# Kernel tuning notes

Hardware: AMD Instinct MI355X
Metric: run time of the kernel (lower is better)

Reference implementation:

```python
import jax, jax.numpy as jnp
import numpy as np

TEMPERATURE = 0.1
N = 8192
V = 2
D = 512

def setup_inputs() -> dict:
    key = jax.random.key(0)
    k1, k2, k3 = jax.random.split(key, 3)
    features = jax.random.normal(k1, (N, V, D), dtype=jnp.float32)
    features1 = jax.random.normal(k2, (N, V, D), dtype=jnp.float32)
    y = jax.random.randint(k3, (N,), 0, 10, dtype=jnp.int64)
    return {"features": features, "features1": features1, "y": y}

def reference(features, features1, y):
    # Take view 0; L2-normalize anchors only (features1 is NOT normalized in the original).
    anchor = features[:, 0, :]
    anchor = anchor / jnp.linalg.norm(anchor, axis=1, keepdims=True)
    f1 = features1[:, 0, :]
    # sim: [N, N]
    sim = jnp.einsum('nd,md->nm', anchor, f1)
    # Original builds logits = [diag_i | row_i without diag] / T and uses label 0.
    # That concat is a permutation of the full row, so
    # CE(row) = logsumexp(row / T) - diag / T, averaged over rows.
    logits = sim / TEMPERATURE
    pos = jnp.diagonal(logits)  # [N]
    loss = jnp.mean(jax.nn.logsumexp(logits, axis=1) - pos)
    return loss
```

## Files before the change

### kernel.cpp

```cpp
#include <hip/hip_runtime.h>
#include <hip/hip_bf16.h>

typedef __attribute__((ext_vector_type(4)))  float f32x4;
typedef __attribute__((ext_vector_type(8)))  int   i32x8;
typedef __attribute__((ext_vector_type(4)))  int   i32x4;

static constexpr int NROW = 8192;
static constexpr int DDIM = 512;
static constexpr float INV_T = 10.0f;
static constexpr float SHIFT = 70.0f;
static constexpr float E2_SC = 14.4269504089f;
static constexpr float E2_BI = -100.988652759f;
static constexpr unsigned SCALE1 = 0x7F7F7F7Fu;

__device__ __forceinline__ void gload_lds16(const void* gsrc, void* ldst) {
  __builtin_amdgcn_global_load_lds(
      (const __attribute__((address_space(1))) unsigned int*)gsrc,
      (__attribute__((address_space(3))) unsigned int*)ldst, 16, 0, 0);
}

__device__ __forceinline__ float fast_exp2(float x) {
#if __has_builtin(__builtin_amdgcn_exp2f)
  return __builtin_amdgcn_exp2f(x);
#else
  float r;
  asm("v_exp_f32 %0, %1" : "=v"(r) : "v"(x));
  return r;
#endif
}

__device__ __forceinline__ unsigned int pack_fp8x4(float x, float y, float z, float w) {
  unsigned int r = 0;
  r = __builtin_amdgcn_cvt_pk_fp8_f32(x, y, r, false);
  r = __builtin_amdgcn_cvt_pk_fp8_f32(z, w, r, true);
  return r;
}

__global__ void prep_kernel(const float* __restrict__ f0,
                            const float* __restrict__ f1,
                            unsigned int* __restrict__ A,
                            unsigned int* __restrict__ B,
                            float* __restrict__ wsS,
                            float* __restrict__ wsPosRow) {
  int gid  = blockIdx.x * blockDim.x + threadIdx.x;
  if (gid < NROW) wsS[gid] = 0.f;
  int wid  = gid >> 6;
  int lane = threadIdx.x & 63;
  const float4* s0 = (const float4*)(f0 + (size_t)wid * (2 * DDIM));
  const float4* s1 = (const float4*)(f1 + (size_t)wid * (2 * DDIM));
  float4 v0 = s0[lane], v1 = s0[lane + 64];
  float4 w0 = s1[lane], w1 = s1[lane + 64];
  float ss = v0.x * v0.x + v0.y * v0.y + v0.z * v0.z + v0.w * v0.w +
             v1.x * v1.x + v1.y * v1.y + v1.z * v1.z + v1.w * v1.w;
  float cc = v0.x * w0.x + v0.y * w0.y + v0.z * w0.z + v0.w * w0.w +
             v1.x * w1.x + v1.y * w1.y + v1.z * w1.z + v1.w * w1.w;
#pragma unroll
  for (int m = 1; m < 64; m <<= 1) {
    ss += __shfl_xor(ss, m);
    cc += __shfl_xor(cc, m);
  }
  float rn = rsqrtf(ss);
  if (lane == 0) wsPosRow[wid] = cc * rn * INV_T;
  A[wid * 128 + lane]      = pack_fp8x4(v0.x * rn, v0.y * rn, v0.z * rn, v0.w * rn);
  A[wid * 128 + 64 + lane] = pack_fp8x4(v1.x * rn, v1.y * rn, v1.z * rn, v1.w * rn);
  B[wid * 128 + lane]      = pack_fp8x4(w0.x, w0.y, w0.z, w0.w);
  B[wid * 128 + 64 + lane] = pack_fp8x4(w1.x, w1.y, w1.z, w1.w);
}

__global__ __launch_bounds__(512, 2) void sim_lse_kernel(
    const unsigned char* __restrict__ Ag,
    const unsigned char* __restrict__ Bg,
    float* __restrict__ wsS) {
  __shared__ __align__(16) char buf0[64 * 512];
  __shared__ __align__(16) char buf1[64 * 512];
  __shared__ __align__(16) char buf2[64 * 512];

  const int tid  = threadIdx.x;
  const int w    = tid >> 6;
  const int lane = tid & 63;
  const int lr   = lane & 15;
  const int kg   = lane >> 4;

  const int p  = blockIdx.x >> 3;
  const int cs = blockIdx.x & 7;
  const int r0 = p * 256 + w * 32;
  const int c0 = cs * 1024;

  const int h5      = lane >> 5;
  const int stg_off = ((lane & 31) << 4) ^ (((2 * w + h5) & 7) << 4);
  const int stg_row = h5;
  const int swz = (lr & 7) << 4;

  i32x8 a0[4], a1[4];
  {
    const char* ar0 = (const char*)Ag + (size_t)(r0 + lr) * DDIM + kg * 32;
    const char* ar1 = (const char*)Ag + (size_t)(r0 + 16 + lr) * DDIM + kg * 32;
#pragma unroll
    for (int ks = 0; ks < 4; ks++) {
      a0[ks] = *(const i32x8*)(ar0 + ks * 128);
      a1[ks] = *(const i32x8*)(ar1 + ks * 128);
    }
  }

  float sums0[4], sums1[4];
#pragma unroll
  for (int r = 0; r < 4; r++) { sums0[r] = 0.f; sums1[r] = 0.f; }

#define STAGE(BUF, T)                                                          \
  {                                                                            \
    const char* gb = (const char*)Bg + (size_t)(c0 + (T) * 64) * DDIM;         \
    _Pragma("unroll")                                                          \
    for (int it = 0; it < 4; it++) {                                           \
      int pr = it * 8 + w;                                                     \
      gload_lds16(gb + (size_t)(2 * pr + stg_row) * DDIM + stg_off,            \
                  (char*)(BUF) + pr * 1024);                                   \
    }                                                                          \
  }

#define MFMA_EPI(BUF)                                                          \
  {                                                                            \
    _Pragma("unroll")                                                          \
    for (int jb = 0; jb < 4; jb++) {                                           \
      const int cb = ((jb * 16 + lr) * 512 + kg * 32) ^ swz;                   \
      const char* p0  = (const char*)(BUF) + cb;                               \
      const char* p0x = (const char*)(BUF) + (cb ^ 16);                        \
      f32x4 acc0 = (f32x4){0.f, 0.f, 0.f, 0.f};                                \
      f32x4 acc1 = (f32x4){0.f, 0.f, 0.f, 0.f};                                \
      __builtin_amdgcn_s_setprio(1);                                           \
      _Pragma("unroll")                                                        \
      for (int ks = 0; ks < 4; ks++) {                                         \
        i32x8 bv = __builtin_shufflevector(                                    \
            *(const i32x4*)(p0 + ks * 128), *(const i32x4*)(p0x + ks * 128),   \
            0, 1, 2, 3, 4, 5, 6, 7);                                           \
        acc0 = __builtin_amdgcn_mfma_scale_f32_16x16x128_f8f6f4(               \
            a0[ks], bv, acc0, 0, 0, 0, SCALE1, 0, SCALE1);                     \
        acc1 = __builtin_amdgcn_mfma_scale_f32_16x16x128_f8f6f4(               \
            a1[ks], bv, acc1, 0, 0, 0, SCALE1, 0, SCALE1);                     \
      }                                                                        \
      __builtin_amdgcn_s_setprio(0);                                           \
      _Pragma("unroll")                                                        \
      for (int r = 0; r < 4; r++) {                                            \
        sums0[r] += fast_exp2(fmaf(acc0[r], E2_SC, E2_BI));                    \
        sums1[r] += fast_exp2(fmaf(acc1[r], E2_SC, E2_BI));                    \
      }                                                                        \
    }                                                                          \
  }

#define WAITBAR4()                                                             \
  {                                                                            \
    asm volatile("s_waitcnt vmcnt(4)" ::: "memory");                           \
    __builtin_amdgcn_s_barrier();                                              \
  }
#define WAITBAR0()                                                             \
  {                                                                            \
    asm volatile("s_waitcnt vmcnt(0)" ::: "memory");                           \
    __builtin_amdgcn_s_barrier();                                              \
  }

  STAGE(buf0, 0);
  STAGE(buf1, 1);
  WAITBAR4();

#pragma unroll 1
  for (int i = 0; i < 4; i++) {
    const int t = 3 * i;
    MFMA_EPI(buf0);  STAGE(buf2, t + 2);  WAITBAR4();
    MFMA_EPI(buf1);  STAGE(buf0, t + 3);  WAITBAR4();
    MFMA_EPI(buf2);  STAGE(buf1, t + 4);  WAITBAR4();
  }
  MFMA_EPI(buf0);  STAGE(buf2, 14);  WAITBAR4();
  MFMA_EPI(buf1);  STAGE(buf0, 15);  WAITBAR4();
  MFMA_EPI(buf2);  WAITBAR0();
  MFMA_EPI(buf0);

#undef STAGE
#undef MFMA_EPI
#undef WAITBAR4
#undef WAITBAR0

#pragma unroll
  for (int r = 0; r < 4; r++) {
    float s0 = sums0[r], s1 = sums1[r];
    s0 += __shfl_xor(s0, 1);  s1 += __shfl_xor(s1, 1);
    s0 += __shfl_xor(s0, 2);  s1 += __shfl_xor(s1, 2);
    s0 += __shfl_xor(s0, 4);  s1 += __shfl_xor(s1, 4);
    s0 += __shfl_xor(s0, 8);  s1 += __shfl_xor(s1, 8);
    if (lr == 0) {
      atomicAdd(&wsS[r0 + kg * 4 + r], s0);
      atomicAdd(&wsS[r0 + 16 + kg * 4 + r], s1);
    }
  }
}

__global__ void finalize_kernel(const float* __restrict__ wsS,
                                const float* __restrict__ wsPosRow,
                                float* __restrict__ out) {
  __shared__ float red[16];
  float part = 0.f;
  for (int r = threadIdx.x; r < NROW; r += 1024)
    part += SHIFT + __logf(wsS[r]) - wsPosRow[r];
#pragma unroll
  for (int m = 1; m < 64; m <<= 1) part += __shfl_xor(part, m);
  if ((threadIdx.x & 63) == 0) red[threadIdx.x >> 6] = part;
  __syncthreads();
  if (threadIdx.x < 16) {
    float t = red[threadIdx.x];
#pragma unroll
    for (int m = 1; m < 16; m <<= 1) t += __shfl_xor(t, m);
    if (threadIdx.x == 0) out[0] = t / (float)NROW;
  }
}

extern "C" void kernel_launch(void* const* d_in, const int* in_sizes, int n_in,
                              void* d_out, int out_size, void* d_ws, size_t ws_size,
                              hipStream_t stream) {
  const float* f0 = (const float*)d_in[0];
  const float* f1 = (const float*)d_in[1];

  unsigned char* A = (unsigned char*)d_ws;
  unsigned char* B = A + (size_t)NROW * DDIM;
  float* wsS      = (float*)(B + (size_t)NROW * DDIM);
  float* wsPosRow = wsS + NROW;

  prep_kernel<<<NROW / 4, 256, 0, stream>>>(f0, f1, (unsigned int*)A,
                                            (unsigned int*)B, wsS, wsPosRow);
  sim_lse_kernel<<<256, 512, 0, stream>>>(A, B, wsS);
  finalize_kernel<<<1, 1024, 0, stream>>>(wsS, wsPosRow, (float*)d_out);
}
```

Baseline: 48.49 us.

## Halve waves per block and give each wave 64 anchor rows

The similarity kernel now runs 4 waves per block instead of 8. Each wave holds 64 anchor rows in registers instead of 32, so every B fragment read from LDS feeds four MFMAs instead of two. Staging is redistributed so each wave issues 8 LDS loads per tile, and the wait count is raised to match. This cuts LDS read traffic per MFMA, at the cost of fewer waves per CU to hide latency and more register pressure.

```diff
diff --git a/kernel.cpp b/kernel.cpp
--- a/kernel.cpp
+++ b/kernel.cpp
@@ -67,7 +67,7 @@
   B[wid * 128 + 64 + lane] = pack_fp8x4(w1.x, w1.y, w1.z, w1.w);
 }
 
-__global__ __launch_bounds__(512, 2) void sim_lse_kernel(
+__global__ __launch_bounds__(256, 1) void sim_lse_kernel(
     const unsigned char* __restrict__ Ag,
     const unsigned char* __restrict__ Bg,
     float* __restrict__ wsS) {
@@ -83,7 +83,7 @@
 
   const int p  = blockIdx.x >> 3;
   const int cs = blockIdx.x & 7;
-  const int r0 = p * 256 + w * 32;
+  const int r0 = p * 256 + w * 64;
   const int c0 = cs * 1024;
 
   const int h5      = lane >> 5;
@@ -91,27 +91,30 @@
   const int stg_row = h5;
   const int swz = (lr & 7) << 4;
 
-  i32x8 a0[4], a1[4];
+  i32x8 a0[4], a1[4], a2[4], a3[4];
   {
-    const char* ar0 = (const char*)Ag + (size_t)(r0 + lr) * DDIM + kg * 32;
-    const char* ar1 = (const char*)Ag + (size_t)(r0 + 16 + lr) * DDIM + kg * 32;
+    const char* base = (const char*)Ag + (size_t)(r0 + lr) * DDIM + kg * 32;
 #pragma unroll
     for (int ks = 0; ks < 4; ks++) {
-      a0[ks] = *(const i32x8*)(ar0 + ks * 128);
-      a1[ks] = *(const i32x8*)(ar1 + ks * 128);
+      a0[ks] = *(const i32x8*)(base + ks * 128);
+      a1[ks] = *(const i32x8*)(base + 16 * DDIM + ks * 128);
+      a2[ks] = *(const i32x8*)(base + 32 * DDIM + ks * 128);
+      a3[ks] = *(const i32x8*)(base + 48 * DDIM + ks * 128);
     }
   }
 
-  float sums0[4], sums1[4];
-#pragma unroll
-  for (int r = 0; r < 4; r++) { sums0[r] = 0.f; sums1[r] = 0.f; }
+  float sums0[4], sums1[4], sums2[4], sums3[4];
+#pragma unroll
+  for (int r = 0; r < 4; r++) {
+    sums0[r] = 0.f; sums1[r] = 0.f; sums2[r] = 0.f; sums3[r] = 0.f;
+  }
 
 #define STAGE(BUF, T)                                                          \
   {                                                                            \
     const char* gb = (const char*)Bg + (size_t)(c0 + (T) * 64) * DDIM;         \
     _Pragma("unroll")                                                          \
-    for (int it = 0; it < 4; it++) {                                           \
-      int pr = it * 8 + w;                                                     \
+    for (int it = 0; it < 8; it++) {                                           \
+      int pr = it * 4 + w;                                                     \
       gload_lds16(gb + (size_t)(2 * pr + stg_row) * DDIM + stg_off,            \
                   (char*)(BUF) + pr * 1024);                                   \
     }                                                                          \
@@ -126,6 +129,8 @@
       const char* p0x = (const char*)(BUF) + (cb ^ 16);                        \
       f32x4 acc0 = (f32x4){0.f, 0.f, 0.f, 0.f};                                \
       f32x4 acc1 = (f32x4){0.f, 0.f, 0.f, 0.f};                                \
+      f32x4 acc2 = (f32x4){0.f, 0.f, 0.f, 0.f};                                \
+      f32x4 acc3 = (f32x4){0.f, 0.f, 0.f, 0.f};                                \
       __builtin_amdgcn_s_setprio(1);                                           \
       _Pragma("unroll")                                                        \
       for (int ks = 0; ks < 4; ks++) {                                         \
@@ -136,19 +141,25 @@
             a0[ks], bv, acc0, 0, 0, 0, SCALE1, 0, SCALE1);                     \
         acc1 = __builtin_amdgcn_mfma_scale_f32_16x16x128_f8f6f4(               \
             a1[ks], bv, acc1, 0, 0, 0, SCALE1, 0, SCALE1);                     \
+        acc2 = __builtin_amdgcn_mfma_scale_f32_16x16x128_f8f6f4(               \
+            a2[ks], bv, acc2, 0, 0, 0, SCALE1, 0, SCALE1);                     \
+        acc3 = __builtin_amdgcn_mfma_scale_f32_16x16x128_f8f6f4(               \
+            a3[ks], bv, acc3, 0, 0, 0, SCALE1, 0, SCALE1);                     \
       }                                                                        \
       __builtin_amdgcn_s_setprio(0);                                           \
       _Pragma("unroll")                                                        \
       for (int r = 0; r < 4; r++) {                                            \
         sums0[r] += fast_exp2(fmaf(acc0[r], E2_SC, E2_BI));                    \
         sums1[r] += fast_exp2(fmaf(acc1[r], E2_SC, E2_BI));                    \
+        sums2[r] += fast_exp2(fmaf(acc2[r], E2_SC, E2_BI));                    \
+        sums3[r] += fast_exp2(fmaf(acc3[r], E2_SC, E2_BI));                    \
       }                                                                        \
     }                                                                          \
   }
 
-#define WAITBAR4()                                                             \
-  {                                                                            \
-    asm volatile("s_waitcnt vmcnt(4)" ::: "memory");                           \
+#define WAITBAR8()                                                             \
+  {                                                                            \
+    asm volatile("s_waitcnt vmcnt(8)" ::: "memory");                           \
     __builtin_amdgcn_s_barrier();                                              \
   }
 #define WAITBAR0()                                                             \
@@ -159,35 +170,41 @@
 
   STAGE(buf0, 0);
   STAGE(buf1, 1);
-  WAITBAR4();
+  WAITBAR8();
 
 #pragma unroll 1
   for (int i = 0; i < 4; i++) {
     const int t = 3 * i;
-    MFMA_EPI(buf0);  STAGE(buf2, t + 2);  WAITBAR4();
-    MFMA_EPI(buf1);  STAGE(buf0, t + 3);  WAITBAR4();
-    MFMA_EPI(buf2);  STAGE(buf1, t + 4);  WAITBAR4();
-  }
-  MFMA_EPI(buf0);  STAGE(buf2, 14);  WAITBAR4();
-  MFMA_EPI(buf1);  STAGE(buf0, 15);  WAITBAR4();
+    MFMA_EPI(buf0);  STAGE(buf2, t + 2);  WAITBAR8();
+    MFMA_EPI(buf1);  STAGE(buf0, t + 3);  WAITBAR8();
+    MFMA_EPI(buf2);  STAGE(buf1, t + 4);  WAITBAR8();
+  }
+  MFMA_EPI(buf0);  STAGE(buf2, 14);  WAITBAR8();
+  MFMA_EPI(buf1);  STAGE(buf0, 15);  WAITBAR8();
   MFMA_EPI(buf2);  WAITBAR0();
   MFMA_EPI(buf0);
 
 #undef STAGE
 #undef MFMA_EPI
-#undef WAITBAR4
+#undef WAITBAR8
 #undef WAITBAR0
 
 #pragma unroll
   for (int r = 0; r < 4; r++) {
-    float s0 = sums0[r], s1 = sums1[r];
+    float s0 = sums0[r], s1 = sums1[r], s2 = sums2[r], s3 = sums3[r];
     s0 += __shfl_xor(s0, 1);  s1 += __shfl_xor(s1, 1);
+    s2 += __shfl_xor(s2, 1);  s3 += __shfl_xor(s3, 1);
     s0 += __shfl_xor(s0, 2);  s1 += __shfl_xor(s1, 2);
+    s2 += __shfl_xor(s2, 2);  s3 += __shfl_xor(s3, 2);
     s0 += __shfl_xor(s0, 4);  s1 += __shfl_xor(s1, 4);
+    s2 += __shfl_xor(s2, 4);  s3 += __shfl_xor(s3, 4);
     s0 += __shfl_xor(s0, 8);  s1 += __shfl_xor(s1, 8);
+    s2 += __shfl_xor(s2, 8);  s3 += __shfl_xor(s3, 8);
     if (lr == 0) {
       atomicAdd(&wsS[r0 + kg * 4 + r], s0);
       atomicAdd(&wsS[r0 + 16 + kg * 4 + r], s1);
+      atomicAdd(&wsS[r0 + 32 + kg * 4 + r], s2);
+      atomicAdd(&wsS[r0 + 48 + kg * 4 + r], s3);
     }
   }
 }
@@ -224,6 +241,6 @@
 
   prep_kernel<<<NROW / 4, 256, 0, stream>>>(f0, f1, (unsigned int*)A,
                                             (unsigned int*)B, wsS, wsPosRow);
-  sim_lse_kernel<<<256, 512, 0, stream>>>(A, B, wsS);
+  sim_lse_kernel<<<256, 256, 0, stream>>>(A, B, wsS);
   finalize_kernel<<<1, 1024, 0, stream>>>(wsS, wsPosRow, (float*)d_out);
 }
```

Result: slower. 58.28 us (+20.2%).
